# Kernel tuning notes

Hardware: AMD Instinct MI355X
Metric: run time of the kernel (lower is better)

The kernel has to match this reference:

```python
import jax, jax.numpy as jnp
import numpy as np

# 7-point Suzuki-Yoshida weights used by the module
_W1 = 0.78451361047756
_W2 = 0.235573213359357
_W3 = -1.17767998417887
_W4 = 1.0 - 2.0 * (_W1 + _W2 + _W3)
SY_WEIGHTS = [_W1, _W2, _W3, _W4, _W3, _W2, _W1]
NRESPA = 2

B, N, D, C = 32, 131072, 3, 5


def setup_inputs() -> dict:
    key = jax.random.key(0)
    k1, k2, k3 = jax.random.split(key, 3)
    return {
        "pos": jax.random.normal(k1, (B, N, D), dtype=jnp.float32),
        "mom": jax.random.normal(k2, (B, N, D), dtype=jnp.float32) * 0.5,
        "mas": jnp.ones((B, N), dtype=jnp.float32),
        "kbt": jnp.ones((B,), dtype=jnp.float32),
        "dtm": jnp.ones((B,), dtype=jnp.float32),
        "pos_nhc": jnp.zeros((B, C), dtype=jnp.float32),
        "mom_nhc": jax.random.normal(k3, (B, C), dtype=jnp.float32) * 0.1,
        "mas_nhc": jnp.ones((B, C), dtype=jnp.float32),
        "stp": jnp.float32(0.002),
    }


def reference(pos, mom, mas, kbt, dtm, pos_nhc, mom_nhc, mas_nhc, stp):
    n_atm, n_dim = pos.shape[1], pos.shape[2]
    nchain = mom_nhc.shape[1]
    dof = jnp.asarray(n_atm * n_dim, dtype=kbt.dtype)  # ddof = 0

    def g_fn(mom_, mom_nhc_):
        # forces on thermostat chain: g[:,0] from atomic KE, g[:,j>0] from chain KE
        kin_nhc = mom_nhc_ * mom_nhc_ / mas_nhc            # [B, C]
        g_rest = kin_nhc[:, :-1] - kbt[:, None]            # [B, C-1]
        g0 = jnp.sum(mom_ * mom_ / mas[:, :, None], axis=(1, 2)) - kbt * dof  # [B]
        return jnp.concatenate([g0[:, None], g_rest], axis=1)  # [B, C]

    def chain_pass(mom_c, g, dea):
        # sequential update down the chain (j = C-2 .. 0); C is small and fixed
        for j in range(nchain - 2, -1, -1):
            f = jnp.exp(-mom_c[:, j + 1] / mas_nhc[:, j + 1] * (dea / 4))
            mom_c = mom_c.at[:, j].set((mom_c[:, j] * f + g[:, j] * (dea / 2)) * f)
        return mom_c

    def substep(mom_, pos_nhc_, mom_nhc_, w):
        dea = dtm * (stp * w / NRESPA)  # [B]
        # First half: g computed from the pre-step chain momenta (constant over loop,
        # matching the original code which never writes mom back into the dict here).
        g = g_fn(mom_, mom_nhc_)
        mc = mom_nhc_.at[:, -1].add(g[:, -1] * (dea / 2))
        mc = chain_pass(mc, g, dea)
        # Drift of chain positions and scaling of atomic momenta
        pos_nhc_ = pos_nhc_ + mc / mas_nhc * dea[:, None]
        mom_ = mom_ * jnp.exp(-mc[:, 0] / mas_nhc[:, 0] * dea)[:, None, None]
        # Second half: g recomputed with the rescaled atomic momenta but the
        # ORIGINAL chain momenta (faithful to the source, which reads out[mom_nhc]
        # from the unmodified dict).
        g2 = g_fn(mom_, mom_nhc_)
        mc = chain_pass(mc, g2, dea)
        mc = mc.at[:, -1].add(g2[:, -1] * (dea / 2))
        return mom_, pos_nhc_, mc

    for _ in range(NRESPA):
        for w in SY_WEIGHTS:
            mom, pos_nhc, mom_nhc = substep(mom, pos_nhc, mom_nhc, w)
    return mom, pos_nhc, mom_nhc
```

## Files before the change

kernel.cpp:

```cpp
#include <hip/hip_runtime.h>

#define NCH 5

__global__ __launch_bounds__(256) void nhc_reduce(
    const float* __restrict__ mom, const float* __restrict__ mas,
    float* __restrict__ partials, int n_atoms, int groups_per_batch,
    int blocks_per_batch)
{
    const int b = blockIdx.y;
    const int t = blockIdx.x * blockDim.x + threadIdx.x;

    float s = 0.0f;
    if (t < groups_per_batch) {
        const float4* mom4 = (const float4*)(mom + (size_t)b * n_atoms * 3);
        const float4* mas4 = (const float4*)(mas + (size_t)b * n_atoms);
        float4 p0 = mom4[3 * t + 0];
        float4 p1 = mom4[3 * t + 1];
        float4 p2 = mom4[3 * t + 2];
        float4 m  = mas4[t];
        s = (p0.x * p0.x + p0.y * p0.y + p0.z * p0.z) / m.x
          + (p0.w * p0.w + p1.x * p1.x + p1.y * p1.y) / m.y
          + (p1.z * p1.z + p1.w * p1.w + p2.x * p2.x) / m.z
          + (p2.y * p2.y + p2.z * p2.z + p2.w * p2.w) / m.w;
    }

    #pragma unroll
    for (int off = 32; off > 0; off >>= 1) s += __shfl_down(s, off, 64);
    __shared__ float lds[4];
    const int lane = threadIdx.x & 63, wv = threadIdx.x >> 6;
    if (lane == 0) lds[wv] = s;
    __syncthreads();
    if (threadIdx.x == 0)
        partials[(size_t)b * blocks_per_batch + blockIdx.x] =
            lds[0] + lds[1] + lds[2] + lds[3];
}

__global__ void nhc_chain(
    const float* __restrict__ partials, int blocks_per_batch,
    const float* __restrict__ kbt, const float* __restrict__ dtm,
    const float* __restrict__ pos_nhc, const float* __restrict__ mom_nhc,
    const float* __restrict__ mas_nhc, const float* __restrict__ stp,
    float* __restrict__ out_posnhc, float* __restrict__ out_momnhc,
    float* __restrict__ scales, int B, float dof)
{
    const int b = blockIdx.x * blockDim.x + threadIdx.x;
    if (b >= B) return;

    float ke = 0.0f;
    for (int i = 0; i < blocks_per_batch; ++i)
        ke += partials[(size_t)b * blocks_per_batch + i];

    constexpr double W1 = 0.78451361047756;
    constexpr double W2 = 0.235573213359357;
    constexpr double W3 = -1.17767998417887;
    constexpr double W4 = 1.0 - 2.0 * (W1 + W2 + W3);
    const float syw[7] = {(float)W1, (float)W2, (float)W3, (float)W4,
                          (float)W3, (float)W2, (float)W1};

    const float kb = kbt[b], dt = dtm[b], st = stp[0];
    float pnh[NCH], mnh[NCH], qn[NCH];
    #pragma unroll
    for (int c = 0; c < NCH; ++c) {
        pnh[c] = pos_nhc[b * NCH + c];
        mnh[c] = mom_nhc[b * NCH + c];
        qn[c]  = mas_nhc[b * NCH + c];
    }

    float Scum = 1.0f;
    for (int r = 0; r < 14; ++r) {
        const float w   = syw[r % 7];
        const float dea = dt * (st * w * 0.5f);
        const float de2 = dea * 0.5f;
        const float de4 = dea * 0.25f;

        float g[NCH], mc[NCH];
        g[0] = ke - kb * dof;
        #pragma unroll
        for (int j = 1; j < NCH; ++j)
            g[j] = mnh[j - 1] * mnh[j - 1] / qn[j - 1] - kb;
        #pragma unroll
        for (int c = 0; c < NCH; ++c) mc[c] = mnh[c];

        mc[NCH - 1] += g[NCH - 1] * de2;
        #pragma unroll
        for (int j = NCH - 2; j >= 0; --j) {
            const float f = expf(-mc[j + 1] / qn[j + 1] * de4);
            mc[j] = (mc[j] * f + g[j] * de2) * f;
        }

        #pragma unroll
        for (int c = 0; c < NCH; ++c) pnh[c] += mc[c] / qn[c] * dea;
        const float s = expf(-mc[0] / qn[0] * dea);
        Scum *= s;
        ke   *= s * s;

        g[0] = ke - kb * dof;
        #pragma unroll
        for (int j = NCH - 2; j >= 0; --j) {
            const float f = expf(-mc[j + 1] / qn[j + 1] * de4);
            mc[j] = (mc[j] * f + g[j] * de2) * f;
        }
        mc[NCH - 1] += g[NCH - 1] * de2;

        #pragma unroll
        for (int c = 0; c < NCH; ++c) mnh[c] = mc[c];
    }

    #pragma unroll
    for (int c = 0; c < NCH; ++c) {
        out_posnhc[b * NCH + c] = pnh[c];
        out_momnhc[b * NCH + c] = mnh[c];
    }
    scales[b] = Scum;
}

__global__ __launch_bounds__(256) void nhc_scale(
    const float* __restrict__ mom, float* __restrict__ out,
    const float* __restrict__ scales, int n4_per_batch)
{
    const int b = blockIdx.y;
    const int i = blockIdx.x * blockDim.x + threadIdx.x;
    if (i >= n4_per_batch) return;
    const float s = scales[b];
    const float4* in4 = (const float4*)mom + (size_t)b * n4_per_batch;
    float4*       o4  = (float4*)out       + (size_t)b * n4_per_batch;
    float4 v = in4[i];
    v.x *= s; v.y *= s; v.z *= s; v.w *= s;
    o4[i] = v;
}

extern "C" void kernel_launch(void* const* d_in, const int* in_sizes, int n_in,
                              void* d_out, int out_size, void* d_ws, size_t ws_size,
                              hipStream_t stream) {
    const float* mom     = (const float*)d_in[1];
    const float* mas     = (const float*)d_in[2];
    const float* kbt     = (const float*)d_in[3];
    const float* dtm     = (const float*)d_in[4];
    const float* pos_nhc = (const float*)d_in[5];
    const float* mom_nhc = (const float*)d_in[6];
    const float* mas_nhc = (const float*)d_in[7];
    const float* stp     = (const float*)d_in[8];

    const int B  = in_sizes[3];
    const int ND = in_sizes[1] / B;
    const int N  = in_sizes[2] / B;
    (void)n_in; (void)ws_size; (void)out_size;
    const float dof = (float)ND;

    const int groups_per_batch = N / 4;
    const int blocks_per_batch = (groups_per_batch + 255) / 256;

    float* partials = (float*)d_ws;
    float* scales   = partials + (size_t)B * blocks_per_batch;

    float* out_f       = (float*)d_out;
    float* out_posnhc  = out_f + (size_t)B * ND;
    float* out_momnhc  = out_posnhc + (size_t)B * NCH;

    nhc_reduce<<<dim3(blocks_per_batch, B), 256, 0, stream>>>(
        mom, mas, partials, N, groups_per_batch, blocks_per_batch);

    nhc_chain<<<1, 64, 0, stream>>>(
        partials, blocks_per_batch, kbt, dtm, pos_nhc, mom_nhc, mas_nhc, stp,
        out_posnhc, out_momnhc, scales, B, dof);

    const int n4 = ND / 4;
    nhc_scale<<<dim3((n4 + 255) / 256, B), 256, 0, stream>>>(
        mom, out_f, scales, n4);
}
```

Measured before the change: 183.6 us.

## Fuse thermostat chain integration into the momentum scaling kernel

Removes the single-block chain kernel and folds it into the scaling kernel. Each block redundantly reduces the per-batch partials with one wavefront, runs the 14-substep chain on lane 0, and shares the scale through LDS. The scale pass then runs as a grid-stride loop over 64 blocks per batch. This saves one launch and the serialized tiny kernel, but every block repeats the serial chain computation before it can scale, and there are fewer blocks for the memory-bound pass.

```diff
diff --git a/kernel.cpp b/kernel.cpp
--- a/kernel.cpp
+++ b/kernel.cpp
@@ -35,98 +35,105 @@
             lds[0] + lds[1] + lds[2] + lds[3];
 }
 
-__global__ void nhc_chain(
-    const float* __restrict__ partials, int blocks_per_batch,
+__global__ __launch_bounds__(256) void nhc_chain_scale(
+    const float* __restrict__ mom, const float* __restrict__ partials,
     const float* __restrict__ kbt, const float* __restrict__ dtm,
     const float* __restrict__ pos_nhc, const float* __restrict__ mom_nhc,
     const float* __restrict__ mas_nhc, const float* __restrict__ stp,
-    float* __restrict__ out_posnhc, float* __restrict__ out_momnhc,
-    float* __restrict__ scales, int B, float dof)
-{
-    const int b = blockIdx.x * blockDim.x + threadIdx.x;
-    if (b >= B) return;
-
-    float ke = 0.0f;
-    for (int i = 0; i < blocks_per_batch; ++i)
-        ke += partials[(size_t)b * blocks_per_batch + i];
-
-    constexpr double W1 = 0.78451361047756;
-    constexpr double W2 = 0.235573213359357;
-    constexpr double W3 = -1.17767998417887;
-    constexpr double W4 = 1.0 - 2.0 * (W1 + W2 + W3);
-    const float syw[7] = {(float)W1, (float)W2, (float)W3, (float)W4,
-                          (float)W3, (float)W2, (float)W1};
-
-    const float kb = kbt[b], dt = dtm[b], st = stp[0];
-    float pnh[NCH], mnh[NCH], qn[NCH];
-    #pragma unroll
-    for (int c = 0; c < NCH; ++c) {
-        pnh[c] = pos_nhc[b * NCH + c];
-        mnh[c] = mom_nhc[b * NCH + c];
-        qn[c]  = mas_nhc[b * NCH + c];
-    }
-
-    float Scum = 1.0f;
-    for (int r = 0; r < 14; ++r) {
-        const float w   = syw[r % 7];
-        const float dea = dt * (st * w * 0.5f);
-        const float de2 = dea * 0.5f;
-        const float de4 = dea * 0.25f;
-
-        float g[NCH], mc[NCH];
-        g[0] = ke - kb * dof;
-        #pragma unroll
-        for (int j = 1; j < NCH; ++j)
-            g[j] = mnh[j - 1] * mnh[j - 1] / qn[j - 1] - kb;
-        #pragma unroll
-        for (int c = 0; c < NCH; ++c) mc[c] = mnh[c];
-
-        mc[NCH - 1] += g[NCH - 1] * de2;
-        #pragma unroll
-        for (int j = NCH - 2; j >= 0; --j) {
-            const float f = expf(-mc[j + 1] / qn[j + 1] * de4);
-            mc[j] = (mc[j] * f + g[j] * de2) * f;
-        }
-
-        #pragma unroll
-        for (int c = 0; c < NCH; ++c) pnh[c] += mc[c] / qn[c] * dea;
-        const float s = expf(-mc[0] / qn[0] * dea);
-        Scum *= s;
-        ke   *= s * s;
-
-        g[0] = ke - kb * dof;
-        #pragma unroll
-        for (int j = NCH - 2; j >= 0; --j) {
-            const float f = expf(-mc[j + 1] / qn[j + 1] * de4);
-            mc[j] = (mc[j] * f + g[j] * de2) * f;
-        }
-        mc[NCH - 1] += g[NCH - 1] * de2;
-
-        #pragma unroll
-        for (int c = 0; c < NCH; ++c) mnh[c] = mc[c];
-    }
-
-    #pragma unroll
-    for (int c = 0; c < NCH; ++c) {
-        out_posnhc[b * NCH + c] = pnh[c];
-        out_momnhc[b * NCH + c] = mnh[c];
-    }
-    scales[b] = Scum;
-}
-
-__global__ __launch_bounds__(256) void nhc_scale(
-    const float* __restrict__ mom, float* __restrict__ out,
-    const float* __restrict__ scales, int n4_per_batch)
+    float* __restrict__ out_mom, float* __restrict__ out_posnhc,
+    float* __restrict__ out_momnhc,
+    int bpb_red, int n4_per_batch, float dof)
 {
     const int b = blockIdx.y;
-    const int i = blockIdx.x * blockDim.x + threadIdx.x;
-    if (i >= n4_per_batch) return;
-    const float s = scales[b];
+    __shared__ float s_scale;
+
+    if (threadIdx.x < 64) {
+        const int lane = threadIdx.x;
+        float ke = 0.0f;
+        for (int i = lane; i < bpb_red; i += 64)
+            ke += partials[(size_t)b * bpb_red + i];
+        #pragma unroll
+        for (int off = 32; off > 0; off >>= 1) ke += __shfl_down(ke, off, 64);
+
+        if (lane == 0) {
+            constexpr double W1 = 0.78451361047756;
+            constexpr double W2 = 0.235573213359357;
+            constexpr double W3 = -1.17767998417887;
+            constexpr double W4 = 1.0 - 2.0 * (W1 + W2 + W3);
+            const float syw[7] = {(float)W1, (float)W2, (float)W3, (float)W4,
+                                  (float)W3, (float)W2, (float)W1};
+
+            const float kb = kbt[b], dt = dtm[b], st = stp[0];
+            float pnh[NCH], mnh[NCH], qn[NCH];
+            #pragma unroll
+            for (int c = 0; c < NCH; ++c) {
+                pnh[c] = pos_nhc[b * NCH + c];
+                mnh[c] = mom_nhc[b * NCH + c];
+                qn[c]  = mas_nhc[b * NCH + c];
+            }
+
+            float Scum = 1.0f;
+            for (int r = 0; r < 14; ++r) {
+                const float w   = syw[r % 7];
+                const float dea = dt * (st * w * 0.5f);
+                const float de2 = dea * 0.5f;
+                const float de4 = dea * 0.25f;
+
+                float g[NCH], mc[NCH];
+                g[0] = ke - kb * dof;
+                #pragma unroll
+                for (int j = 1; j < NCH; ++j)
+                    g[j] = mnh[j - 1] * mnh[j - 1] / qn[j - 1] - kb;
+                #pragma unroll
+                for (int c = 0; c < NCH; ++c) mc[c] = mnh[c];
+
+                mc[NCH - 1] += g[NCH - 1] * de2;
+                #pragma unroll
+                for (int j = NCH - 2; j >= 0; --j) {
+                    const float f = expf(-mc[j + 1] / qn[j + 1] * de4);
+                    mc[j] = (mc[j] * f + g[j] * de2) * f;
+                }
+
+                #pragma unroll
+                for (int c = 0; c < NCH; ++c) pnh[c] += mc[c] / qn[c] * dea;
+                const float s = expf(-mc[0] / qn[0] * dea);
+                Scum *= s;
+                ke   *= s * s;
+
+                g[0] = ke - kb * dof;
+                #pragma unroll
+                for (int j = NCH - 2; j >= 0; --j) {
+                    const float f = expf(-mc[j + 1] / qn[j + 1] * de4);
+                    mc[j] = (mc[j] * f + g[j] * de2) * f;
+                }
+                mc[NCH - 1] += g[NCH - 1] * de2;
+
+                #pragma unroll
+                for (int c = 0; c < NCH; ++c) mnh[c] = mc[c];
+            }
+
+            s_scale = Scum;
+            if (blockIdx.x == 0) {
+                #pragma unroll
+                for (int c = 0; c < NCH; ++c) {
+                    out_posnhc[b * NCH + c] = pnh[c];
+                    out_momnhc[b * NCH + c] = mnh[c];
+                }
+            }
+        }
+    }
+    __syncthreads();
+
+    const float s = s_scale;
     const float4* in4 = (const float4*)mom + (size_t)b * n4_per_batch;
-    float4*       o4  = (float4*)out       + (size_t)b * n4_per_batch;
-    float4 v = in4[i];
-    v.x *= s; v.y *= s; v.z *= s; v.w *= s;
-    o4[i] = v;
+    float4*       o4  = (float4*)out_mom   + (size_t)b * n4_per_batch;
+    const int stride = gridDim.x * blockDim.x;
+    for (int i = blockIdx.x * blockDim.x + threadIdx.x; i < n4_per_batch;
+         i += stride) {
+        float4 v = in4[i];
+        v.x *= s; v.y *= s; v.z *= s; v.w *= s;
+        o4[i] = v;
+    }
 }
 
 extern "C" void kernel_launch(void* const* d_in, const int* in_sizes, int n_in,
@@ -151,7 +158,6 @@
     const int blocks_per_batch = (groups_per_batch + 255) / 256;
 
     float* partials = (float*)d_ws;
-    float* scales   = partials + (size_t)B * blocks_per_batch;
 
     float* out_f       = (float*)d_out;
     float* out_posnhc  = out_f + (size_t)B * ND;
@@ -160,11 +166,8 @@
     nhc_reduce<<<dim3(blocks_per_batch, B), 256, 0, stream>>>(
         mom, mas, partials, N, groups_per_batch, blocks_per_batch);
 
-    nhc_chain<<<1, 64, 0, stream>>>(
-        partials, blocks_per_batch, kbt, dtm, pos_nhc, mom_nhc, mas_nhc, stp,
-        out_posnhc, out_momnhc, scales, B, dof);
-
     const int n4 = ND / 4;
-    nhc_scale<<<dim3((n4 + 255) / 256, B), 256, 0, stream>>>(
-        mom, out_f, scales, n4);
+    nhc_chain_scale<<<dim3(64, B), 256, 0, stream>>>(
+        mom, partials, kbt, dtm, pos_nhc, mom_nhc, mas_nhc, stp,
+        out_f, out_posnhc, out_momnhc, blocks_per_batch, n4, dof);
 }
```

Result: faster. 178.2 us (-2.9%).
